# Kernel optimization log

Measured on AMD Instinct MI355X. Metric: run time of the kernel, lower is better.

Reference implementation:

```python
import jax, jax.numpy as jnp
from jax import lax
import numpy as np

WINDOW = 7
SIGMA = 1.5
DATA_RANGE = 2.0
SSIM_WEIGHT = 0.5
VQ_WEIGHT = 1.0
FG_WEIGHT = 5.0
BG_THRESHOLD = -0.9


def _gaussian_1d(dtype=jnp.float32):
    coords = jnp.arange(WINDOW, dtype=dtype) - (WINDOW - 1) / 2.0
    g = jnp.exp(-coords ** 2 / (2.0 * SIGMA ** 2))
    return g / g.sum()


def _blur3d(x, g):
    # Separable gaussian blur == dense 7x7x7 gaussian conv (kernel is an outer product).
    # x: (B,1,D,H,W); three 1D passes along D, H, W with SAME (zero) padding.
    dn = ('NCDHW', 'OIDHW', 'NCDHW')
    for shape in [(1, 1, WINDOW, 1, 1), (1, 1, 1, WINDOW, 1), (1, 1, 1, 1, WINDOW)]:
        x = lax.conv_general_dilated(x, g.reshape(shape), (1, 1, 1), 'SAME',
                                     dimension_numbers=dn)
    return x


def ssim3d(x, y):
    C1 = (0.01 * DATA_RANGE) ** 2
    C2 = (0.03 * DATA_RANGE) ** 2
    g = _gaussian_1d(x.dtype)
    mu_x = _blur3d(x, g)
    mu_y = _blur3d(y, g)
    mu_x2, mu_y2, mu_xy = mu_x * mu_x, mu_y * mu_y, mu_x * mu_y
    sigma_x2 = _blur3d(x * x, g) - mu_x2
    sigma_y2 = _blur3d(y * y, g) - mu_y2
    sigma_xy = _blur3d(x * y, g) - mu_xy
    ssim_map = (2 * mu_xy + C1) * (2 * sigma_xy + C2) / (
        (mu_x2 + mu_y2 + C1) * (sigma_x2 + sigma_y2 + C2))
    return ssim_map.mean()


def weighted_l1(recon, target):
    w = jnp.where(target > BG_THRESHOLD, FG_WEIGHT, 1.0).astype(recon.dtype)
    return jnp.sum(w * jnp.abs(recon - target)) / jnp.sum(w)


def setup_inputs() -> dict:
    key = jax.random.key(0)
    k1, k2, k3 = jax.random.split(key, 3)
    shape = (4, 1, 160, 192, 192)
    recon = jax.random.normal(k1, shape, dtype=jnp.float32)
    target = jax.random.normal(k2, shape, dtype=jnp.float32)
    vq_loss = jax.random.uniform(k3, (), dtype=jnp.float32)
    return {"recon": recon, "target": target, "vq_loss": vq_loss}


def reference(recon, target, vq_loss):
    l1 = weighted_l1(recon, target)
    ssim_term = 1.0 - ssim3d(recon.astype(jnp.float32), target.astype(jnp.float32))
    rec = l1 + SSIM_WEIGHT * ssim_term
    total = rec + VQ_WEIGHT * vq_loss
    return total
```

## Files before the change

### kernel.cpp

```cpp
#include <hip/hip_runtime.h>
#include <math.h>

typedef __attribute__((ext_vector_type(2))) float f32x2;
typedef __attribute__((ext_vector_type(4))) float f32x4;

#define BDIM 4
#define DDIM 160
#define HDIM 192
#define WDIM 192
#define NTOT (BDIM * DDIM * HDIM * WDIM)
#define SLICEPX (HDIM * WDIM)

template<int N> struct IC { static constexpr int v = N; };

__device__ __forceinline__ float rcp_fast(float x) {
#if __has_builtin(__builtin_amdgcn_rcpf)
    return __builtin_amdgcn_rcpf(x);
#else
    return 1.0f / x;
#endif
}

__device__ __forceinline__ unsigned bfr(float f) {
    unsigned u = __float_as_uint(f);
    return (u + 0x7fffu + ((u >> 16) & 1u)) >> 16;
}

#define G7INIT { 0.03663285f, 0.11128076f, 0.21674532f, 0.27068215f, \
                 0.21674532f, 0.11128076f, 0.03663285f }

#define STEP_BARRIER() do {                                   \
    asm volatile("s_waitcnt lgkmcnt(0)" ::: "memory");        \
    __builtin_amdgcn_s_barrier();                             \
} while (0)

#define ATH 8
#define ARH 14
#define HBW 200
#define NSL 166
#define SPB 8

struct PFBuf { f32x4 x0, y0, x1, y1; };

__global__ __launch_bounds__(512, 4)
void nq_fields(const float* __restrict__ X, const float* __restrict__ Y,
               uint2* __restrict__ F, float2* __restrict__ pl1)
{
    constexpr float Gc[7] = G7INIT;
    __shared__ __align__(16) f32x2 raw[ARH][WDIM];
    __shared__ __align__(16) f32x2 hA[ATH][HBW];
    __shared__ __align__(16) f32x2 hB[ATH][HBW];
    __shared__ float red[8][2];

    const int t = threadIdx.x;
    const int strip = blockIdx.x;
    const int z = blockIdx.z;
    const int h0 = strip * ATH;
    const int b0 = blockIdx.y * SPB;

    const int r0 = t / 48, c0 = (t % 48) * 4;
    const int h0r0 = h0 + r0 - 3;
    const bool okh0 = (unsigned)h0r0 < (unsigned)HDIM;
    const bool int0 = (r0 >= 3) && (r0 < 11);
    const int off0 = h0r0 * WDIM + c0;
    const int lof0 = r0 * WDIM + c0;

    const bool act1 = t < 160;
    const int i4b = 512 + t;
    const int r1 = i4b / 48, c1 = (i4b % 48) * 4;
    const int h0r1 = h0 + r1 - 3;
    const bool okh1 = act1 && ((unsigned)h0r1 < (unsigned)HDIM);
    const bool int1 = act1 && (r1 >= 3) && (r1 < 11);
    const int off1 = h0r1 * WDIM + c1;
    const int lof1 = r1 * WDIM + c1;

    const int hr0 = t / 96,        hw0 = (t % 96) * 2;
    const int hr1 = (t + 512) / 96, hw1 = ((t + 512) % 96) * 2;
    const bool hact1 = t < 256;

    if (t < 64) {
        const int r = t >> 3, c8 = t & 7;
        const int col = (c8 < 4) ? c8 : (192 + c8 - 4 + 4);
        hA[r][col] = (f32x2){0.f, 0.f};
        hB[r][col] = (f32x2){0.f, 0.f};
    }

    float l1n = 0.f, l1d = 0.f;
    PFBuf pfA, pfB;

    auto validby = [&](int by) { return (by >= 3) && (by < 163); };

    auto issue = [&](PFBuf& p, int by) {
        const int d = by - 3;
        const size_t sbase = ((size_t)z * DDIM + d) * SLICEPX;
        const f32x4 zz = {0.f, 0.f, 0.f, 0.f};
        p.x0 = okh0 ? *(const f32x4*)(X + sbase + off0) : zz;
        p.y0 = okh0 ? *(const f32x4*)(Y + sbase + off0) : zz;
        p.x1 = okh1 ? *(const f32x4*)(X + sbase + off1) : zz;
        p.y1 = okh1 ? *(const f32x4*)(Y + sbase + off1) : zz;
    };

    auto commit = [&](PFBuf& p) {
        if (int0) {
            #pragma unroll
            for (int j = 0; j < 4; ++j) {
                const float x = p.x0[j], y = p.y0[j];
                const float wgt = (y > -0.9f) ? 5.f : 1.f;
                l1n += wgt * fabsf(x - y);
                l1d += wgt;
            }
        }
        if (int1) {
            #pragma unroll
            for (int j = 0; j < 4; ++j) {
                const float x = p.x1[j], y = p.y1[j];
                const float wgt = (y > -0.9f) ? 5.f : 1.f;
                l1n += wgt * fabsf(x - y);
                l1d += wgt;
            }
        }
        f32x2* r = &raw[0][0];
        *(f32x4*)(r + lof0)     = (f32x4){p.x0.x + p.y0.x, p.x0.x - p.y0.x,
                                          p.x0.y + p.y0.y, p.x0.y - p.y0.y};
        *(f32x4*)(r + lof0 + 2) = (f32x4){p.x0.z + p.y0.z, p.x0.z - p.y0.z,
                                          p.x0.w + p.y0.w, p.x0.w - p.y0.w};
        if (act1) {
            *(f32x4*)(r + lof1)     = (f32x4){p.x1.x + p.y1.x, p.x1.x - p.y1.x,
                                              p.x1.y + p.y1.y, p.x1.y - p.y1.y};
            *(f32x4*)(r + lof1 + 2) = (f32x4){p.x1.z + p.y1.z, p.x1.z - p.y1.z,
                                              p.x1.w + p.y1.w, p.x1.w - p.y1.w};
        }
    };

    auto hitem = [&](int r, int w0) {
        f32x2 aA0 = {0.f, 0.f}, aA1 = {0.f, 0.f};
        f32x2 aB0 = {0.f, 0.f}, aB1 = {0.f, 0.f};
        #pragma unroll
        for (int k = 0; k < 7; ++k) {
            const f32x4 v = *(const f32x4*)(&raw[r + k][w0]);
            const f32x2 p0 = {v.x, v.y}, p1 = {v.z, v.w};
            const float g = Gc[k];
            aA0 += g * p0; aB0 += (g * p0) * p0;
            aA1 += g * p1; aB1 += (g * p1) * p1;
        }
        *(f32x4*)(&hA[r][4 + w0]) = (f32x4){aA0.x, aA0.y, aA1.x, aA1.y};
        *(f32x4*)(&hB[r][4 + w0]) = (f32x4){aB0.x, aB0.y, aB1.x, aB1.y};
    };

    auto wstore = [&](int by) {
        const size_t obase = ((size_t)z * NSL + by) * SLICEPX;
        #pragma unroll
        for (int j = 0; j < 3; ++j) {
            const int px = t + j * 512;
            const int r = px / WDIM, w = px - r * WDIM;
            f32x2 a = {0.f, 0.f}, e = {0.f, 0.f};
            #pragma unroll
            for (int k = 0; k < 7; ++k) {
                const float g = Gc[k];
                a += g * hA[r][w + 1 + k];
                e += g * hB[r][w + 1 + k];
            }
            uint2 o;
            o.x = bfr(a.x) | (bfr(a.y) << 16);
            o.y = bfr(e.x) | (bfr(e.y) << 16);
            F[obase + (size_t)(h0 + r) * WDIM + w] = o;
        }
    };

    if (validby(b0))     { issue(pfB, b0); commit(pfB); }
    if (validby(b0 + 1)) issue(pfB, b0 + 1);
    STEP_BARRIER();

    auto iter = [&](auto ICi) {
        constexpr int i = ICi.v;
        const int c = b0 + i;
        PFBuf& ld = (i % 2 == 0) ? pfA : pfB;
        PFBuf& cm = (i % 2 == 0) ? pfB : pfA;
        if (validby(c + 2)) issue(ld, c + 2);
        if (validby(c)) {
            hitem(hr0, hw0);
            if (hact1) hitem(hr1, hw1);
        }
        STEP_BARRIER();
        if (validby(c)) wstore(c);
        if (validby(c + 1)) commit(cm);
        STEP_BARRIER();
    };
    iter(IC<0>{}); iter(IC<1>{}); iter(IC<2>{}); iter(IC<3>{});
    iter(IC<4>{}); iter(IC<5>{}); iter(IC<6>{}); iter(IC<7>{});

    #pragma unroll
    for (int off = 32; off > 0; off >>= 1) {
        l1n += __shfl_down(l1n, off, 64);
        l1d += __shfl_down(l1d, off, 64);
    }
    const int wave = t >> 6, lane = t & 63;
    if (lane == 0) { red[wave][0] = l1n; red[wave][1] = l1d; }
    __syncthreads();
    if (t == 0) {
        float n = 0.f, dn = 0.f;
        #pragma unroll
        for (int i2 = 0; i2 < 8; ++i2) { n += red[i2][0]; dn += red[i2][1]; }
        const int bidx = (z * gridDim.y + blockIdx.y) * gridDim.x + blockIdx.x;
        pl1[bidx] = (float2){n, dn};
    }
}

__global__ __launch_bounds__(512, 4)
void nq_ssim(const uint2* __restrict__ F, float* __restrict__ pssim)
{
    constexpr float Gc[7] = G7INIT;
    constexpr float C1f = 4.0e-4f;
    constexpr float C2f = 3.6e-3f;
    __shared__ float red[8];

    const int t = threadIdx.x;
    const int p = blockIdx.x * 512 + t;
    const int gd0 = blockIdx.y * 20;
    const size_t fb = (size_t)blockIdx.z * NSL * SLICEPX;

    float ssum = 0.f;
    f32x2 wM[7], wE[7];

    auto loadF = [&](int ds) -> uint2 {
        const int di = gd0 - 3 + ds;
        if ((unsigned)di < (unsigned)DDIM)
            return F[fb + (size_t)(di + 3) * SLICEPX + p];
        return (uint2){0u, 0u};
    };

    uint2 nf = loadF(0);

    auto step = [&](auto PPc, int it) {
        constexpr int PP = PPc.v;
        const int ds = it * 7 + PP;
        if (ds < 26) {
            const uint2 cur = nf;
            if (ds + 1 < 26) nf = loadF(ds + 1);
            wM[PP] = (f32x2){__uint_as_float(cur.x << 16),
                             __uint_as_float(cur.x & 0xffff0000u)};
            wE[PP] = (f32x2){__uint_as_float(cur.y << 16),
                             __uint_as_float(cur.y & 0xffff0000u)};
            if (ds >= 6) {
                f32x2 mu = {0.f, 0.f}, e2 = {0.f, 0.f};
                #pragma unroll
                for (int k = 0; k < 7; ++k) {
                    const int s = (PP + 1 + k) % 7;
                    const float g = Gc[k];
                    mu += g * wM[s]; e2 += g * wE[s];
                }
                const float P = mu.x * mu.x, Q = mu.y * mu.y;
                const float u_ = 0.5f * (P + Q);
                const float v_ = 0.5f * (P - Q);
                const float a2 = 0.5f * (e2.x + e2.y);
                const float b2 = 0.5f * (e2.x - e2.y);
                const float num = (v_ + C1f) * (b2 - v_ + C2f);
                const float den = (u_ + C1f) * (a2 - u_ + C2f);
                ssum += num * rcp_fast(den);
            }
        }
    };

    for (int it = 0; it < 4; ++it) {
        step(IC<0>{}, it); step(IC<1>{}, it); step(IC<2>{}, it);
        step(IC<3>{}, it); step(IC<4>{}, it); step(IC<5>{}, it);
        step(IC<6>{}, it);
    }

    #pragma unroll
    for (int off = 32; off > 0; off >>= 1) ssum += __shfl_down(ssum, off, 64);
    const int wave = t >> 6, lane = t & 63;
    if (lane == 0) red[wave] = ssum;
    __syncthreads();
    if (t == 0) {
        float s = 0.f;
        #pragma unroll
        for (int i = 0; i < 8; ++i) s += red[i];
        pssim[(blockIdx.z * gridDim.y + blockIdx.y) * gridDim.x + blockIdx.x] = s;
    }
}

__global__ void nq_reduce(const float* __restrict__ pssim, int nss,
                          const float2* __restrict__ pl1, int nl1,
                          const float* __restrict__ vq, float* __restrict__ out)
{
    __shared__ float red[4][3];
    const int t = threadIdx.x;
    float s = 0.f, n = 0.f, dn = 0.f;
    for (int i = t; i < nss; i += 256) s += pssim[i];
    for (int i = t; i < nl1; i += 256) { const float2 v = pl1[i]; n += v.x; dn += v.y; }
    #pragma unroll
    for (int off = 32; off > 0; off >>= 1) {
        s  += __shfl_down(s,  off, 64);
        n  += __shfl_down(n,  off, 64);
        dn += __shfl_down(dn, off, 64);
    }
    const int wave = t >> 6, lane = t & 63;
    if (lane == 0) { red[wave][0] = s; red[wave][1] = n; red[wave][2] = dn; }
    __syncthreads();
    if (t == 0) {
        float S = 0.f, N = 0.f, DN = 0.f;
        #pragma unroll
        for (int i = 0; i < 4; ++i) { S += red[i][0]; N += red[i][1]; DN += red[i][2]; }
        out[0] = N / DN + 0.5f * (1.0f - S / (float)NTOT) + vq[0];
    }
}

#define TH 8
#define TW 64
#define SEG 20
#define NSEG (DDIM / SEG)
#define NS  (SEG + 6)
#define NTH 512
#define RHH (TH + 6)
#define RWW 70
#define NRAW (RHH * RWW)
#define HBSTR 72

__global__ __launch_bounds__(NTH, 4)
void nq_mono(const float* __restrict__ X, const float* __restrict__ Y,
             float* __restrict__ acc)
{
    constexpr float Gc[7] = G7INIT;
    constexpr float C1f = 4.0e-4f;
    constexpr float C2f = 3.6e-3f;

    __shared__ __align__(16) f32x2 raw[2][NRAW];
    __shared__ __align__(16) f32x2 hbA[2][TH][HBSTR];
    __shared__ __align__(16) f32x2 hbB[2][TH][HBSTR];
    __shared__ float red[NTH / 64][3];

    const int wt  = blockIdx.x;
    const int ht  = blockIdx.y;
    const int b   = blockIdx.z >> 3;
    const int seg = blockIdx.z & 7;
    const int h0 = ht * TH, w0 = wt * TW;
    const int dbase = seg * SEG;
    const long long bbase = (long long)b * (DDIM * HDIM * WDIM);
    const int t = threadIdx.x;

    int goff[2]; bool ok[2], inter[2];
    #pragma unroll
    for (int i = 0; i < 2; ++i) {
        const int idx = t + i * NTH;
        const int hh = idx / RWW, ww = idx - hh * RWW;
        const int h = h0 + hh - 3, w = w0 + ww - 3;
        bool o_ = ((unsigned)h < HDIM) && ((unsigned)w < WDIM);
        bool in_ = ((unsigned)(hh - 3) < TH) && ((unsigned)(ww - 3) < TW);
        if (i == 1 && idx >= NRAW) { o_ = false; in_ = false; }
        ok[i] = o_; inter[i] = in_;
        goff[i] = h * WDIM + w;
    }
    const bool has1 = (t + NTH) < NRAW;

    const int q0r = t / RWW,         q0w = t - q0r * RWW;
    const int q1r = (t + NTH) / RWW, q1w = (t + NTH) - q1r * RWW;
    const bool q1on = t < (TH * RWW - NTH);

    const int p4r = t >> 6;
    const int p4c = t & 63;

    float ssum = 0.f, l1n = 0.f, l1d = 0.f;
    f32x2 wA[7], wB[7];
    float pfs[2], pfd[2];

    auto loadslice = [&](int s) {
        const int d_g = dbase - 3 + s;
        const bool dok = (unsigned)d_g < (unsigned)DDIM;
        const long long sb = bbase + (long long)d_g * (HDIM * WDIM);
        const bool l1on = (s >= 3) && (s <= SEG + 2);
        #pragma unroll
        for (int i = 0; i < 2; ++i) {
            const bool l = dok && ok[i];
            const float xv = l ? X[sb + goff[i]] : 0.f;
            const float yv = l ? Y[sb + goff[i]] : 0.f;
            if (l1on && inter[i]) {
                const float wgt = (yv > -0.9f) ? 5.f : 1.f;
                l1n += wgt * fabsf(xv - yv);
                l1d += wgt;
            }
            pfs[i] = xv + yv;
            pfd[i] = xv - yv;
        }
    };

    auto commit = [&](int s) {
        const int rb = s & 1;
        raw[rb][t] = (f32x2){pfs[0], pfd[0]};
        if (has1) raw[rb][t + NTH] = (f32x2){pfs[1], pfd[1]};
    };

    auto p2item = [&](int rb, int r, int w) {
        f32x2 aA = {0.f, 0.f}, aB = {0.f, 0.f};
        #pragma unroll
        for (int k = 0; k < 7; ++k) {
            const f32x2 p = raw[rb][(r + k) * RWW + w];
            const float g = Gc[k];
            aA += g * p;
            aB += (g * p) * p;
        }
        hbA[rb][r][w] = aA;
        hbB[rb][r][w] = aB;
    };

    auto phase = [&](auto PPc, int it) {
        constexpr int PP = PPc.v;
        constexpr int SLOT = (PP + 6) % 7;
        const int ps = it * 7 + PP;
        const int par = ps & 1;

        if (ps <= NS - 2) commit(ps + 1);
        if (ps <= NS - 3) loadslice(ps + 2);

        if (ps <= NS - 1) {
            p2item(par, q0r, q0w);
            if (q1on) p2item(par, q1r, q1w);
        }
        if (ps >= 1 && ps <= NS) {
            const int hp = par ^ 1;
            f32x2 a = {0.f, 0.f}, bv = {0.f, 0.f};
            #pragma unroll
            for (int k = 0; k < 7; ++k) {
                const float g = Gc[k];
                a  += g * hbA[hp][p4r][p4c + k];
                bv += g * hbB[hp][p4r][p4c + k];
            }
            wA[SLOT] = a; wB[SLOT] = bv;
            if (ps >= 7) {
                f32x2 mu = {0.f, 0.f}, e2 = {0.f, 0.f};
                #pragma unroll
                for (int k = 0; k < 7; ++k) {
                    const int s = (PP + k) % 7;
                    const float g = Gc[k];
                    mu += g * wA[s]; e2 += g * wB[s];
                }
                const float P = mu.x * mu.x, Q = mu.y * mu.y;
                const float u  = 0.5f * (P + Q);
                const float v_ = 0.5f * (P - Q);
                const float a2 = 0.5f * (e2.x + e2.y);
                const float b2 = 0.5f * (e2.x - e2.y);
                const float num = (v_ + C1f) * (b2 - v_ + C2f);
                const float den = (u  + C1f) * (a2 - u  + C2f);
                ssum += num * rcp_fast(den);
            }
        }
        __syncthreads();
    };

    loadslice(0);
    commit(0);
    loadslice(1);
    __syncthreads();

    for (int it = 0; it < 4; ++it) {
        phase(IC<0>{}, it); phase(IC<1>{}, it); phase(IC<2>{}, it);
        phase(IC<3>{}, it); phase(IC<4>{}, it); phase(IC<5>{}, it);
        phase(IC<6>{}, it);
    }

    #pragma unroll
    for (int off = 32; off > 0; off >>= 1) {
        ssum += __shfl_down(ssum, off, 64);
        l1n  += __shfl_down(l1n,  off, 64);
        l1d  += __shfl_down(l1d,  off, 64);
    }
    const int wave = t >> 6, lane = t & 63;
    if (lane == 0) { red[wave][0] = ssum; red[wave][1] = l1n; red[wave][2] = l1d; }
    __syncthreads();
    if (t == 0) {
        float s = 0.f, n = 0.f, dn = 0.f;
        #pragma unroll
        for (int i = 0; i < NTH / 64; ++i) {
            s += red[i][0]; n += red[i][1]; dn += red[i][2];
        }
        atomicAdd(&acc[0], s);
        atomicAdd(&acc[1], n);
        atomicAdd(&acc[2], dn);
    }
}

__global__ void nq_final_acc(const float* __restrict__ acc,
                             const float* __restrict__ vq,
                             float* __restrict__ out)
{
    const float ssim_mean = acc[0] / (float)NTOT;
    out[0] = acc[1] / acc[2] + 0.5f * (1.0f - ssim_mean) + vq[0];
}

extern "C" void kernel_launch(void* const* d_in, const int* in_sizes, int n_in,
                              void* d_out, int out_size, void* d_ws, size_t ws_size,
                              hipStream_t stream)
{
    const float* X  = (const float*)d_in[0];
    const float* Y  = (const float*)d_in[1];
    const float* vq = (const float*)d_in[2];
    float* out = (float*)d_out;

    const size_t needFull = 256 + (size_t)BDIM * NSL * SLICEPX * 8;

    if (ws_size >= needFull) {
        uint2* F = (uint2*)((char*)d_ws + 256);
        char* tail = (char*)d_ws + 256 + (size_t)(3 * NSL + 163) * SLICEPX * 8;
        float*  pssim = (float*)tail;
        float2* pl1   = (float2*)(tail + 16384);

        nq_fields<<<dim3(24, 21, 4), 512, 0, stream>>>(X, Y, F, pl1);
        nq_ssim  <<<dim3(72, 8, 4),  512, 0, stream>>>(F, pssim);
        nq_reduce<<<1, 256, 0, stream>>>(pssim, 2304, pl1, 2016, vq, out);
    } else {
        float* acc = (float*)d_ws;
        hipMemsetAsync(acc, 0, 16, stream);
        nq_mono<<<dim3(WDIM / TW, HDIM / TH, BDIM * NSEG), NTH, 0, stream>>>(X, Y, acc);
        nq_final_acc<<<1, 1, 0, stream>>>(acc, vq, out);
    }
}
```

Before: 159.4 us.

## Halve slices per block and vectorize W-pass with register reuse and 16B stores

```diff
diff --git a/kernel.cpp b/kernel.cpp
--- a/kernel.cpp
+++ b/kernel.cpp
@@ -38,7 +38,7 @@
 #define ARH 14
 #define HBW 200
 #define NSL 166
-#define SPB 8
+#define SPB 4
 
 struct PFBuf { f32x4 x0, y0, x1, y1; };
 
@@ -74,13 +74,16 @@
     const int off1 = h0r1 * WDIM + c1;
     const int lof1 = r1 * WDIM + c1;
 
-    const int hr0 = t / 96,        hw0 = (t % 96) * 2;
+    const int hr0 = t / 96,         hw0 = (t % 96) * 2;
     const int hr1 = (t + 512) / 96, hw1 = ((t + 512) % 96) * 2;
     const bool hact1 = t < 256;
 
+    const int wr0 = t / 96,         ww0 = (t % 96) * 2;
+    const int wr1 = (t + 512) / 96, ww1 = ((t + 512) % 96) * 2;
+
     if (t < 64) {
         const int r = t >> 3, c8 = t & 7;
-        const int col = (c8 < 4) ? c8 : (192 + c8 - 4 + 4);
+        const int col = (c8 < 4) ? c8 : (192 + c8);
         hA[r][col] = (f32x2){0.f, 0.f};
         hB[r][col] = (f32x2){0.f, 0.f};
     }
@@ -147,24 +150,35 @@
         *(f32x4*)(&hB[r][4 + w0]) = (f32x4){aB0.x, aB0.y, aB1.x, aB1.y};
     };
 
+    auto witem = [&](int r, int w0, size_t obase) {
+        f32x2 vA[10], vB[10];
+        #pragma unroll
+        for (int j = 0; j < 5; ++j) {
+            const f32x4 qa = *(const f32x4*)(&hA[r][w0 + 2 * j]);
+            vA[2 * j] = (f32x2){qa.x, qa.y}; vA[2 * j + 1] = (f32x2){qa.z, qa.w};
+            const f32x4 qb = *(const f32x4*)(&hB[r][w0 + 2 * j]);
+            vB[2 * j] = (f32x2){qb.x, qb.y}; vB[2 * j + 1] = (f32x2){qb.z, qb.w};
+        }
+        f32x2 a0 = {0.f, 0.f}, a1 = {0.f, 0.f};
+        f32x2 e0 = {0.f, 0.f}, e1 = {0.f, 0.f};
+        #pragma unroll
+        for (int k = 0; k < 7; ++k) {
+            const float g = Gc[k];
+            a0 += g * vA[1 + k]; a1 += g * vA[2 + k];
+            e0 += g * vB[1 + k]; e1 += g * vB[2 + k];
+        }
+        uint4 o;
+        o.x = bfr(a0.x) | (bfr(a0.y) << 16);
+        o.y = bfr(e0.x) | (bfr(e0.y) << 16);
+        o.z = bfr(a1.x) | (bfr(a1.y) << 16);
+        o.w = bfr(e1.x) | (bfr(e1.y) << 16);
+        *(uint4*)&F[obase + (size_t)(h0 + r) * WDIM + w0] = o;
+    };
+
     auto wstore = [&](int by) {
         const size_t obase = ((size_t)z * NSL + by) * SLICEPX;
-        #pragma unroll
-        for (int j = 0; j < 3; ++j) {
-            const int px = t + j * 512;
-            const int r = px / WDIM, w = px - r * WDIM;
-            f32x2 a = {0.f, 0.f}, e = {0.f, 0.f};
-            #pragma unroll
-            for (int k = 0; k < 7; ++k) {
-                const float g = Gc[k];
-                a += g * hA[r][w + 1 + k];
-                e += g * hB[r][w + 1 + k];
-            }
-            uint2 o;
-            o.x = bfr(a.x) | (bfr(a.y) << 16);
-            o.y = bfr(e.x) | (bfr(e.y) << 16);
-            F[obase + (size_t)(h0 + r) * WDIM + w] = o;
-        }
+        witem(wr0, ww0, obase);
+        if (hact1) witem(wr1, ww1, obase);
     };
 
     if (validby(b0))     { issue(pfB, b0); commit(pfB); }
@@ -187,7 +201,6 @@
         STEP_BARRIER();
     };
     iter(IC<0>{}); iter(IC<1>{}); iter(IC<2>{}); iter(IC<3>{});
-    iter(IC<4>{}); iter(IC<5>{}); iter(IC<6>{}); iter(IC<7>{});
 
     #pragma unroll
     for (int off = 32; off > 0; off >>= 1) {
@@ -504,9 +517,9 @@
         float*  pssim = (float*)tail;
         float2* pl1   = (float2*)(tail + 16384);
 
-        nq_fields<<<dim3(24, 21, 4), 512, 0, stream>>>(X, Y, F, pl1);
+        nq_fields<<<dim3(24, 42, 4), 512, 0, stream>>>(X, Y, F, pl1);
         nq_ssim  <<<dim3(72, 8, 4),  512, 0, stream>>>(F, pssim);
-        nq_reduce<<<1, 256, 0, stream>>>(pssim, 2304, pl1, 2016, vq, out);
+        nq_reduce<<<1, 256, 0, stream>>>(pssim, 2304, pl1, 4032, vq, out);
     } else {
         float* acc = (float*)d_ws;
         hipMemsetAsync(acc, 0, 16, stream);
```

New measurement: 142.7 us. -10.5%, faster.
